# Kernel tuning notes

Hardware: AMD Instinct MI355X
Metric: run time of the kernel (lower is better)

Reference implementation:

```python
import jax, jax.numpy as jnp
import numpy as np

V = 50257   # vocab_size
E = 300     # embedding_dim
H2 = 1024   # hidden_size*2
CH = 6      # char_num
PMR = 32    # pmr_size
SX = 8192   # encoded_x seq len
SC = 4096   # encoded_con seq len
B = 1       # batch (decode step assumes b=1, see argmax/.item() in source)
S = 0.05    # weight init scale


def setup_inputs() -> dict:
    key = jax.random.key(0)
    ks = jax.random.split(key, 20)
    return {
        'input_idx': jax.random.randint(ks[0], (B,), 0, V),
        'encoded_x': jax.random.normal(ks[1], (B, SX, H2), jnp.float32),
        'encoded_con': jax.random.normal(ks[2], (B, SC, H2), jnp.float32),
        'p_matrix': jax.random.normal(ks[3], (B, CH * PMR, H2), jnp.float32),
        'hid': jax.random.normal(ks[4], (1, B, H2), jnp.float32),
        'c': jax.random.normal(ks[5], (1, B, H2), jnp.float32),
        'mask_x': jnp.ones((B, SX), bool),
        'mask_c': jnp.ones((B, SC), bool),
        # learned parameters
        'embed': jax.random.normal(ks[6], (V, E)) * S,
        'Wa': jax.random.normal(ks[7], (2 * H2, H2)) * S,   # Bahdanau attn proj
        'ba': jnp.zeros((H2,)),
        'va': jax.random.normal(ks[8], (H2,)) * S,
        'Wg': jax.random.normal(ks[9], (2 * H2, H2)) * S,   # fc_gate1
        'bg': jnp.zeros((H2,)),
        'Wchar': jax.random.normal(ks[10], (E + 2 * H2, CH)) * S,
        'bchar': jnp.zeros((CH,)),
        'Wp': jax.random.normal(ks[11], (H2, H2)) * S,       # w_p
        'bp': jnp.zeros((H2,)),
        'Wh': jax.random.normal(ks[12], (H2, H2)) * S,       # w_h
        'bh': jnp.zeros((H2,)),
        'vv': jax.random.normal(ks[13], (H2,)) * S,          # v (no bias)
        'Wy': jax.random.normal(ks[14], (E + 2 * H2, E)) * S,  # y_inp
        'by': jnp.zeros((E,)),
        'Wih': jax.random.normal(ks[15], (E, 4 * H2)) * S,   # LSTM input weights (i,f,g,o)
        'Whh': jax.random.normal(ks[16], (H2, 4 * H2)) * S,
        'bih': jnp.zeros((4 * H2,)),
        'bhh': jnp.zeros((4 * H2,)),
        'Wout': jax.random.normal(ks[17], (H2, V)) * S,      # out2
        'bout': jnp.zeros((V,)),
    }


def reference(input_idx, encoded_x, encoded_con, p_matrix, hid, c, mask_x, mask_c,
              embed, Wa, ba, va, Wg, bg, Wchar, bchar, Wp, bp, Wh, bh, vv,
              Wy, by, Wih, Whh, bih, bhh, Wout, bout):
    b = input_idx.shape[0]
    h0 = hid[0]                    # [b, 2h]
    c0 = c[0]
    y_input = embed[input_idx]     # [b, e] (dropout is identity at eval)

    def bahdanau(h, enc, mask):
        # h: [b,2h], enc: [b,seq,2h], mask: [b,seq] -> softmax weights [b,seq]
        hrep = jnp.broadcast_to(h[:, None, :], enc.shape)
        energy = jnp.tanh(jnp.concatenate([hrep, enc], -1) @ Wa + ba)  # [b,seq,2h]
        scores = energy @ va                                          # [b,seq]
        scores = jnp.where(mask, scores, -1e10)
        return jax.nn.softmax(scores, axis=1)

    a_x = bahdanau(h0, encoded_x, mask_x)
    weighted_x = jnp.einsum('bs,bsd->bd', a_x, encoded_x)
    a_c = bahdanau(h0, encoded_con, mask_c)
    weighted_c = jnp.einsum('bs,bsd->bd', a_c, encoded_con)
    weighted = jnp.concatenate([weighted_x, weighted_c], -1) @ Wg + bg  # [b,2h]

    # pointer: soft gate over chars -> hard one-hot selection -> gather rows of p_matrix
    g_char = jax.nn.softmax(jnp.concatenate([y_input, h0, weighted], -1) @ Wchar + bchar, axis=1)  # [b,6]
    pm = p_matrix.reshape(b, CH, -1)                       # [b,6,pmr*2h]
    nz = (pm.sum(axis=2) != 0).astype(g_char.dtype)
    z_char = g_char * nz
    o_char = jax.nn.one_hot(jnp.argmax(z_char, axis=1), CH, dtype=z_char.dtype)  # [b,6]
    s_char = (o_char[:, :, None] * pm).reshape(b, CH * PMR, H2)                  # [b,192,2h]

    # additive attention over the 192 selected slots (replicates source repeat/view layout, valid for b=1)
    hh = jnp.tile(h0, (CH * PMR, 1))                       # [192*b, 2h]
    pp = (s_char @ Wp + bp).reshape(-1, H2)                # [b*192, 2h]
    att = jnp.tanh(hh @ Wh + bh + pp) @ vv                 # [192*b]
    p_attn_score = jax.nn.softmax(att.reshape(b, -1), axis=1)     # [b,192]
    p_attn = jnp.einsum('bn,bnd->bd', p_attn_score, s_char)       # [b,2h]
    ps6 = p_attn_score.reshape(CH, -1)                            # [6, b*32]
    sel = jnp.argmax(o_char.reshape(-1))
    p_attn_score_sel = jnp.take(ps6, sel, axis=0)[None, :]        # [1, b*32]

    # LSTM cell step (torch gate order i,f,g,o)
    y_in = jnp.concatenate([y_input, weighted, p_attn], -1) @ Wy + by  # [b,e]
    gates = y_in @ Wih + bih + h0 @ Whh + bhh                          # [b,8h]
    gi, gf, gg, go = jnp.split(gates, 4, axis=1)
    c1 = jax.nn.sigmoid(gf) * c0 + jax.nn.sigmoid(gi) * jnp.tanh(gg)
    h1 = jax.nn.sigmoid(go) * jnp.tanh(c1)

    out = jax.nn.softmax(h1 @ Wout + bout, axis=1)[:, None, :]  # [b,1,vocab]
    return (out, h1[None], c1[None], weighted[:, None, :], p_attn_score_sel)
```

## Files before the change

kernel.cpp:

```cpp
#include <hip/hip_runtime.h>
#include <hip/hip_bf16.h>
#include <math.h>

typedef short short8 __attribute__((ext_vector_type(8)));
typedef float f32x4 __attribute__((ext_vector_type(4)));

#define DEV static __device__ __forceinline__

DEV void gl2lds16(const void* g, void* l) {
  __builtin_amdgcn_global_load_lds(
      (const __attribute__((address_space(1))) unsigned int*)g,
      (__attribute__((address_space(3))) unsigned int*)l, 16, 0, 0);
}

DEV float wred_sum(float v) {
#pragma unroll
  for (int o = 1; o < 64; o <<= 1) v += __shfl_xor(v, o, 64);
  return v;
}
DEV float wred_max(float v) {
#pragma unroll
  for (int o = 1; o < 64; o <<= 1) v = fmaxf(v, __shfl_xor(v, o, 64));
  return v;
}
DEV float sigmoidf(float x) { return 1.0f / (1.0f + expf(-x)); }

DEV unsigned short f2bf(float x) {
  unsigned u = __float_as_uint(x);
  unsigned rr = (u + 0x7fffu + ((u >> 16) & 1u)) >> 16;
  return (unsigned short)rr;
}

DEV short8 cvt8(float4 f0, float4 f1) {
  union { short8 s; unsigned u[4]; } r;
  asm("v_cvt_pk_bf16_f32 %0, %1, %2" : "=v"(r.u[0]) : "v"(f0.x), "v"(f0.y));
  asm("v_cvt_pk_bf16_f32 %0, %1, %2" : "=v"(r.u[1]) : "v"(f0.z), "v"(f0.w));
  asm("v_cvt_pk_bf16_f32 %0, %1, %2" : "=v"(r.u[2]) : "v"(f1.x), "v"(f1.y));
  asm("v_cvt_pk_bf16_f32 %0, %1, %2" : "=v"(r.u[3]) : "v"(f1.z), "v"(f1.w));
  return r.s;
}

#define OUT_H1 50257
#define OUT_C1 51281
#define OUT_W  52305
#define OUT_PS 53329

__global__ void k_prep_bT(const float* __restrict__ Wa, unsigned short* __restrict__ WaT) {
  __shared__ float tile[64][65];
  int bi = blockIdx.x, bj = blockIdx.y, t = threadIdx.x;
  int c = t & 63, rq = t >> 6;
#pragma unroll
  for (int rr = 0; rr < 16; rr++) {
    int kl = rr * 4 + rq;
    tile[kl][c] = Wa[(size_t)(1024 + bi * 64 + kl) * 1024 + bj * 64 + c];
  }
  __syncthreads();
#pragma unroll
  for (int rr = 0; rr < 16; rr++) {
    int nl = rr * 4 + rq;
    WaT[(size_t)(bj * 64 + nl) * 1024 + bi * 64 + c] = f2bf(tile[c][nl]);
  }
}

__global__ void k_prep_small(const float* __restrict__ Wa, const float* __restrict__ ba,
                             const float* __restrict__ Wh, const float* __restrict__ bh,
                             const float* __restrict__ hid, const float* __restrict__ embed,
                             const int* __restrict__ idx, const float* __restrict__ pmat,
                             float* __restrict__ hWa, float* __restrict__ hWh,
                             float* __restrict__ yinp, float* __restrict__ nz) {
  __shared__ float red[8][64];
  __shared__ float r2[8];
  int bx = blockIdx.x, t = threadIdx.x;
  if (bx < 32) {
    int ol = t & 63, kc = t >> 6;
    int o = bx * 64 + ol;
    const float* W = (o < 1024) ? Wa : Wh;
    int col = (o < 1024) ? o : (o - 1024);
    float acc = 0.f;
#pragma unroll 4
    for (int k = kc * 128; k < kc * 128 + 128; k++) acc += hid[k] * W[(size_t)k * 1024 + col];
    red[kc][ol] = acc;
    __syncthreads();
    if (t < 64) {
      int oo = bx * 64 + t;
      float s = 0.f;
#pragma unroll
      for (int q = 0; q < 8; q++) s += red[q][t];
      if (oo < 1024) hWa[oo] = s + ba[oo];
      else hWh[oo - 1024] = s + bh[oo - 1024];
    }
  } else if (bx == 32) {
    int id = idx[0];
    for (int k = t; k < 300; k += 512) yinp[k] = embed[(size_t)id * 300 + k];
  } else {
    int j = bx - 33;
    float a = 0.f;
    for (int k = t; k < 32768; k += 512) a += pmat[(size_t)j * 32768 + k];
    a = wred_sum(a);
    if ((t & 63) == 0) r2[t >> 6] = a;
    __syncthreads();
    if (t == 0) {
      float s = 0.f;
#pragma unroll
      for (int q = 0; q < 8; q++) s += r2[q];
      nz[j] = s;
    }
  }
}

__global__ __launch_bounds__(256) void k_scores_gemm(
    const float* __restrict__ ex, const float* __restrict__ ec,
    const unsigned short* __restrict__ WaT, const float* __restrict__ hWa,
    const float* __restrict__ va, float* __restrict__ scoresP) {
  __shared__ __align__(16) float As[128 * 32];
  __shared__ __align__(16) unsigned short Bs[128 * 32];
  __shared__ float red[2][128];
  int mtile = blockIdx.x, ntile = blockIdx.y;
  int t = threadIdx.x, lane = t & 63, wid = t >> 6;
  int wr = wid >> 1, wc = wid & 1;
  int l15 = lane & 15, lg = lane >> 4;
  int r0 = mtile * 128;
  const float* Asrc = (r0 < 8192) ? (ex + (size_t)r0 * 1024) : (ec + (size_t)(r0 - 8192) * 1024);

  f32x4 acc[4][4];
#pragma unroll
  for (int m = 0; m < 4; m++)
#pragma unroll
    for (int n = 0; n < 4; n++) acc[m][n] = (f32x4){0.f, 0.f, 0.f, 0.f};

  for (int kt = 0; kt < 1024; kt += 32) {
#pragma unroll
    for (int p = 0; p < 4; p++) {
      int cb = p * 256 + wid * 64;
      int c = cb + lane;
      const float* g = Asrc + (size_t)(c >> 3) * 1024 + kt + (c & 7) * 4;
      gl2lds16(g, &As[cb * 4]);
    }
#pragma unroll
    for (int p = 0; p < 2; p++) {
      int cb = p * 256 + wid * 64;
      int c = cb + lane;
      const unsigned short* g = WaT + (size_t)(ntile * 128 + (c >> 2)) * 1024 + kt + (c & 3) * 8;
      gl2lds16(g, &Bs[cb * 8]);
    }
    __syncthreads();
    short8 a[4], b[4];
#pragma unroll
    for (int m = 0; m < 4; m++) {
      const float* ap = &As[(wr * 64 + m * 16 + l15) * 32 + lg * 8];
      float4 f0 = *(const float4*)ap;
      float4 f1 = *(const float4*)(ap + 4);
      a[m] = cvt8(f0, f1);
    }
#pragma unroll
    for (int n = 0; n < 4; n++)
      b[n] = *(const short8*)&Bs[(wc * 64 + n * 16 + l15) * 32 + lg * 8];
#pragma unroll
    for (int m = 0; m < 4; m++)
#pragma unroll
      for (int n = 0; n < 4; n++)
        acc[m][n] = __builtin_amdgcn_mfma_f32_16x16x32_bf16(a[m], b[n], acc[m][n], 0, 0, 0);
    __syncthreads();
  }

  float vva[4], hba[4];
#pragma unroll
  for (int n = 0; n < 4; n++) {
    int col = ntile * 128 + wc * 64 + n * 16 + l15;
    vva[n] = va[col];
    hba[n] = hWa[col];
  }
#pragma unroll
  for (int m = 0; m < 4; m++) {
#pragma unroll
    for (int j = 0; j < 4; j++) {
      float p = 0.f;
#pragma unroll
      for (int n = 0; n < 4; n++) p += vva[n] * tanhf(acc[m][n][j] + hba[n]);
#pragma unroll
      for (int o = 1; o < 16; o <<= 1) p += __shfl_xor(p, o, 64);
      if (l15 == 0) red[wc][wr * 64 + m * 16 + lg * 4 + j] = p;
    }
  }
  __syncthreads();
  if (t < 128) scoresP[(size_t)ntile * 12288 + r0 + t] = red[0][t] + red[1][t];
}

__global__ void k_scores_reduce(const float* __restrict__ scoresP, float* __restrict__ scores,
                                float* __restrict__ bmax, float* __restrict__ bz) {
  __shared__ float r4[4];
  int bx = blockIdx.x, t = threadIdx.x;
  int r = bx * 256 + t;
  float s = 0.f;
#pragma unroll
  for (int nt = 0; nt < 8; nt++) s += scoresP[(size_t)nt * 12288 + r];
  scores[r] = s;
  float m = wred_max(s);
  if ((t & 63) == 0) r4[t >> 6] = m;
  __syncthreads();
  m = fmaxf(fmaxf(r4[0], r4[1]), fmaxf(r4[2], r4[3]));
  __syncthreads();
  float z = expf(s - m);
  z = wred_sum(z);
  if ((t & 63) == 0) r4[t >> 6] = z;
  __syncthreads();
  if (t == 0) { bmax[bx] = m; bz[bx] = r4[0] + r4[1] + r4[2] + r4[3]; }
}

__global__ void k_weighted_part(const float* __restrict__ ex, const float* __restrict__ ec,
                                const float* __restrict__ scores, const float* __restrict__ bmax,
                                const float* __restrict__ bz, float* __restrict__ partw) {
  __shared__ float wrow[64];
  int b = blockIdx.x, colq = blockIdx.y, t = threadIdx.x;
  int seg = (b >= 128) ? 1 : 0;
  int rb = (seg ? (b - 128) : b) * 64;
  int sbase = seg ? 8192 : 0;
  if (t < 64) {
    int b0 = seg ? 32 : 0, cnt = seg ? 16 : 32;
    float mv = (t < cnt) ? bmax[b0 + t] : -1e30f;
    float m = wred_max(mv);
    float zv = (t < cnt) ? bz[b0 + t] * expf(bmax[b0 + t] - m) : 0.f;
    float z = wred_sum(zv);
    wrow[t] = expf(scores[sbase + rb + t] - m) / z;
  }
  __syncthreads();
  const float* src = seg ? ec : ex;
  int col = colq * 256 + t;
  float acc = 0.f;
#pragma unroll 8
  for (int r = 0; r < 64; r++) acc += wrow[r] * src[(size_t)(rb + r) * 1024 + col];
  partw[(size_t)b * 1024 + col] = acc;
}

__global__ void k_weighted_combine(const float* __restrict__ partw, float* __restrict__ wxc) {
  int d = blockIdx.x * 256 + threadIdx.x;
  float sx = 0.f, sc = 0.f;
#pragma unroll 8
  for (int b = 0; b < 128; b++) sx += partw[(size_t)b * 1024 + d];
#pragma unroll 8
  for (int b = 128; b < 192; b++) sc += partw[(size_t)b * 1024 + d];
  wxc[d] = sx; wxc[1024 + d] = sc;
}

__global__ void k_weighted_gemv(const float* __restrict__ wxc, const float* __restrict__ Wg,
                                float* __restrict__ wgP) {
  int o = blockIdx.x * 256 + threadIdx.x;
  int kb = blockIdx.y * 64;
  float acc = 0.f;
#pragma unroll 8
  for (int k = kb; k < kb + 64; k++) acc += wxc[k] * Wg[(size_t)k * 1024 + o];
  wgP[(size_t)blockIdx.y * 1024 + o] = acc;
}

__global__ void k_wgfin_charsel(const float* __restrict__ wgP, const float* __restrict__ bg,
                                const float* __restrict__ yinp, const float* __restrict__ hid,
                                const float* __restrict__ Wchar, const float* __restrict__ bchar,
                                const float* __restrict__ nz, float* __restrict__ weighted,
                                int* __restrict__ sel, float* __restrict__ dout) {
  __shared__ float WL[1024];
  __shared__ float red[4][6];
  int t = threadIdx.x;
  for (int q = 0; q < 4; q++) {
    int d = t + q * 256;
    float s = bg[d];
#pragma unroll 8
    for (int b = 0; b < 32; b++) s += wgP[(size_t)b * 1024 + d];
    WL[d] = s;
    weighted[d] = s;
    dout[OUT_W + d] = s;
  }
  __syncthreads();
  float p[6] = {0.f, 0.f, 0.f, 0.f, 0.f, 0.f};
  for (int k = t; k < 2348; k += 256) {
    float xv = (k < 300) ? yinp[k] : (k < 1324 ? hid[k - 300] : WL[k - 1324]);
#pragma unroll
    for (int ch = 0; ch < 6; ch++) p[ch] += xv * Wchar[k * 6 + ch];
  }
#pragma unroll
  for (int ch = 0; ch < 6; ch++) {
    float v = wred_sum(p[ch]);
    if ((t & 63) == 0) red[t >> 6][ch] = v;
  }
  __syncthreads();
  if (t == 0) {
    float best = -1e30f; int si = 0;
    for (int ch = 0; ch < 6; ch++) {
      float lgt = red[0][ch] + red[1][ch] + red[2][ch] + red[3][ch] + bchar[ch];
      if (nz[ch] != 0.0f && lgt > best) { best = lgt; si = ch; }
    }
    *sel = si;
  }
}

__global__ void k_pp(const float* __restrict__ pmat, const float* __restrict__ Wp,
                     const int* __restrict__ sel, float* __restrict__ ppP) {
  __shared__ float sr[32][64];
  int oq = blockIdx.x, kq = blockIdx.y, t = threadIdx.x;
  int row0 = (*sel) * 32;
  int k0 = kq * 64;
#pragma unroll
  for (int j = 0; j < 8; j++) {
    int idx = t + j * 256;
    int i = idx >> 6, kk = idx & 63;
    sr[i][kk] = pmat[(size_t)(row0 + i) * 1024 + k0 + kk];
  }
  __syncthreads();
  int o = oq * 256 + t;
  float acc[32];
#pragma unroll
  for (int i = 0; i < 32; i++) acc[i] = 0.f;
  for (int k = 0; k < 64; k++) {
    float w = Wp[(size_t)(k0 + k) * 1024 + o];
#pragma unroll
    for (int i = 0; i < 32; i++) acc[i] += sr[i][k] * w;
  }
#pragma unroll
  for (int i = 0; i < 32; i++) ppP[(size_t)kq * 32768 + i * 1024 + o] = acc[i];
}

__global__ void k_pp_fin(const float* __restrict__ ppP, const float* __restrict__ bp,
                         float* __restrict__ pp) {
  int i = blockIdx.x, t = threadIdx.x;
  for (int q = 0; q < 4; q++) {
    int d = t + q * 256;
    float s = bp[d];
#pragma unroll
    for (int kq = 0; kq < 16; kq++) s += ppP[(size_t)kq * 32768 + i * 1024 + d];
    pp[i * 1024 + d] = s;
  }
}

__global__ void k_att(const float* __restrict__ pp, const float* __restrict__ hWh,
                      const float* __restrict__ bp, const float* __restrict__ vv,
                      float* __restrict__ attb) {
  __shared__ float r4[4];
  int i = blockIdx.x, t = threadIdx.x;
  const float* src = (i < 32) ? (pp + i * 1024) : bp;
  float pt = 0.f;
  for (int n = t; n < 1024; n += 256) pt += vv[n] * tanhf(hWh[n] + src[n]);
  pt = wred_sum(pt);
  if ((t & 63) == 0) r4[t >> 6] = pt;
  __syncthreads();
  if (t == 0) attb[i] = r4[0] + r4[1] + r4[2] + r4[3];
}

__global__ void k_pattn2(const float* __restrict__ attb, const float* __restrict__ pmat,
                         const int* __restrict__ sel, float* __restrict__ pattn,
                         float* __restrict__ dout) {
  __shared__ float sc32[32];
  int t = threadIdx.x, bx = blockIdx.x;
  if (t == 0) {
    float az = attb[32];
    float m = az;
    for (int i = 0; i < 32; i++) m = fmaxf(m, attb[i]);
    float Z = 160.0f * expf(az - m);
    for (int i = 0; i < 32; i++) Z += expf(attb[i] - m);
    for (int i = 0; i < 32; i++) sc32[i] = expf(attb[i] - m) / Z;
  }
  __syncthreads();
  if (bx == 0 && t < 32) dout[OUT_PS + t] = sc32[t];
  int d = bx * 256 + t;
  int srow0 = (*sel) * 32;
  float acc = 0.f;
#pragma unroll
  for (int i = 0; i < 32; i++) acc += sc32[i] * pmat[(size_t)(srow0 + i) * 1024 + d];
  pattn[d] = acc;
}

__global__ void k_yin_part(const float* __restrict__ yinp, const float* __restrict__ weighted,
                           const float* __restrict__ pattn, const float* __restrict__ Wy,
                           float* __restrict__ yinP) {
  __shared__ float XLb[74];
  int b = blockIdx.x, t = threadIdx.x;
  int base = b * 74;
  int len = 2348 - base; if (len > 74) len = 74;
  if (t < len) {
    int k = base + t;
    XLb[t] = (k < 300) ? yinp[k] : (k < 1324 ? weighted[k - 300] : pattn[k - 1324]);
  }
  __syncthreads();
  if (t < 300) {
    float acc = 0.f;
    for (int j = 0; j < len; j++) acc += XLb[j] * Wy[(size_t)(base + j) * 300 + t];
    yinP[b * 300 + t] = acc;
  }
}

__global__ void k_gates_part(const float* __restrict__ yinP, const float* __restrict__ by,
                             const float* __restrict__ hid,
                             const float* __restrict__ Wih, const float* __restrict__ Whh,
                             float* __restrict__ gatesP) {
  __shared__ float YLb[40];
  __shared__ float red[4][64];
  int bx = blockIdx.x, kq = blockIdx.y, t = threadIdx.x;
  int k0i = kq * 38;
  int k1i = k0i + 38; if (k1i > 300) k1i = 300;
  if (t < k1i - k0i) {
    float s = by[k0i + t];
#pragma unroll 8
    for (int b = 0; b < 32; b++) s += yinP[b * 300 + k0i + t];
    YLb[t] = s;
  }
  __syncthreads();
  int ol = t & 63, kc = t >> 6;
  int o = bx * 64 + ol;
  float acc = 0.f;
  for (int k = k0i + kc; k < k1i; k += 4) acc += YLb[k - k0i] * Wih[(size_t)k * 4096 + o];
  int kh0 = kq * 128;
#pragma unroll 4
  for (int k = kh0 + kc; k < kh0 + 128; k += 4) acc += hid[k] * Whh[(size_t)k * 4096 + o];
  red[kc][ol] = acc;
  __syncthreads();
  if (t < 64) {
    int oo = bx * 64 + t;
    gatesP[(size_t)kq * 4096 + oo] = red[0][t] + red[1][t] + red[2][t] + red[3][t];
  }
}

__global__ void k_lstm(const float* __restrict__ gatesP, const float* __restrict__ bih,
                       const float* __restrict__ bhh, const float* __restrict__ c0,
                       float* __restrict__ h1ws, float* __restrict__ dout) {
  int t = threadIdx.x;
  for (int q = 0; q < 4; q++) {
    int d = t + q * 256;
    float gi = bih[d] + bhh[d];
    float gf = bih[1024 + d] + bhh[1024 + d];
    float gg = bih[2048 + d] + bhh[2048 + d];
    float go = bih[3072 + d] + bhh[3072 + d];
#pragma unroll
    for (int kq = 0; kq < 8; kq++) {
      const float* g = gatesP + (size_t)kq * 4096;
      gi += g[d]; gf += g[1024 + d]; gg += g[2048 + d]; go += g[3072 + d];
    }
    float c1 = sigmoidf(gf) * c0[d] + sigmoidf(gi) * tanhf(gg);
    float h1 = sigmoidf(go) * tanhf(c1);
    h1ws[d] = h1;
    dout[OUT_H1 + d] = h1;
    dout[OUT_C1 + d] = c1;
  }
}

__global__ __launch_bounds__(256) void k_out_gemv(const float* __restrict__ h1,
                                                  const float* __restrict__ Wout,
                                                  float* __restrict__ partK) {
  __shared__ float hh[64];
  int ks = blockIdx.x, cb = blockIdx.y, t = threadIdx.x;
  if (t < 64) hh[t] = h1[ks * 64 + t];
  __syncthreads();
  int c0 = cb * 512 + t;
  int c1 = c0 + 256;
  bool v0 = c0 < 50257, v1 = c1 < 50257;
  float a0 = 0.f, a1 = 0.f;
  const float* W = Wout + (size_t)ks * 64 * 50257;
#pragma unroll 8
  for (int k = 0; k < 64; k++) {
    const float* row = W + (size_t)k * 50257;
    float h = hh[k];
    if (v0) a0 += h * row[c0];
    if (v1) a1 += h * row[c1];
  }
  float* dst = partK + (size_t)ks * 50257;
  if (v0) dst[c0] = a0;
  if (v1) dst[c1] = a1;
}

__global__ void k_logits_stats(const float* __restrict__ partK, const float* __restrict__ bout,
                               float* __restrict__ logits, float* __restrict__ bstat) {
  __shared__ float r4[4];
  int bx = blockIdx.x, t = threadIdx.x;
  int c = bx * 256 + t;
  float v = -1e30f;
  if (c < 50257) {
    v = bout[c];
#pragma unroll
    for (int ks = 0; ks < 16; ks++) v += partK[(size_t)ks * 50257 + c];
    logits[c] = v;
  }
  float m = wred_max(v);
  if ((t & 63) == 0) r4[t >> 6] = m;
  __syncthreads();
  m = fmaxf(fmaxf(r4[0], r4[1]), fmaxf(r4[2], r4[3]));
  __syncthreads();
  float z = (c < 50257) ? expf(v - m) : 0.f;
  z = wred_sum(z);
  if ((t & 63) == 0) r4[t >> 6] = z;
  __syncthreads();
  if (t == 0) { bstat[bx] = m; bstat[256 + bx] = r4[0] + r4[1] + r4[2] + r4[3]; }
}

__global__ void k_out_final(const float* __restrict__ bstat, const float* __restrict__ logits,
                            float* __restrict__ dout) {
  __shared__ float r4m[4], r4z[4];
  int bx = blockIdx.x, t = threadIdx.x;
  float mv = (t < 197) ? bstat[t] : -1e30f;
  float m = wred_max(mv);
  if ((t & 63) == 0) r4m[t >> 6] = m;
  __syncthreads();
  m = fmaxf(fmaxf(r4m[0], r4m[1]), fmaxf(r4m[2], r4m[3]));
  __syncthreads();
  float zv = (t < 197) ? bstat[256 + t] * expf(bstat[t] - m) : 0.f;
  float z = wred_sum(zv);
  if ((t & 63) == 0) r4z[t >> 6] = z;
  __syncthreads();
  float Z = r4z[0] + r4z[1] + r4z[2] + r4z[3];
  int c = bx * 256 + t;
  if (c < 50257) dout[c] = expf(logits[c] - m) / Z;
}

extern "C" void kernel_launch(void* const* d_in, const int* in_sizes, int n_in,
                              void* d_out, int out_size, void* d_ws, size_t ws_size,
                              hipStream_t stream) {
  (void)in_sizes; (void)n_in; (void)out_size; (void)ws_size;
  const int*   idx   = (const int*)  d_in[0];
  const float* ex    = (const float*)d_in[1];
  const float* ec    = (const float*)d_in[2];
  const float* pmat  = (const float*)d_in[3];
  const float* hid   = (const float*)d_in[4];
  const float* c0    = (const float*)d_in[5];
  const float* embed = (const float*)d_in[8];
  const float* Wa    = (const float*)d_in[9];
  const float* ba    = (const float*)d_in[10];
  const float* va    = (const float*)d_in[11];
  const float* Wg    = (const float*)d_in[12];
  const float* bg    = (const float*)d_in[13];
  const float* Wchar = (const float*)d_in[14];
  const float* bchar = (const float*)d_in[15];
  const float* Wp    = (const float*)d_in[16];
  const float* bp    = (const float*)d_in[17];
  const float* Wh    = (const float*)d_in[18];
  const float* bh    = (const float*)d_in[19];
  const float* vv    = (const float*)d_in[20];
  const float* Wy    = (const float*)d_in[21];
  const float* by    = (const float*)d_in[22];
  const float* Wih   = (const float*)d_in[23];
  const float* Whh   = (const float*)d_in[24];
  const float* bih   = (const float*)d_in[25];
  const float* bhh   = (const float*)d_in[26];
  const float* Wout  = (const float*)d_in[27];
  const float* bout  = (const float*)d_in[28];
  float* out = (float*)d_out;

  char* ws = (char*)d_ws;
  unsigned short* WaT = (unsigned short*)(ws + 0);
  float* scoresP  = (float*)(ws + 2097152);
  float* scores   = (float*)(ws + 2490368);
  float* bmax     = (float*)(ws + 2539520);
  float* bz       = (float*)(ws + 2539776);
  float* partw    = (float*)(ws + 2540032);
  float* wxc      = (float*)(ws + 3326464);
  float* wgP      = (float*)(ws + 3334656);
  float* partK    = (float*)(ws + 0);
  float* logits   = (float*)(ws + 3216640);
  float* pp       = (float*)(ws + 3465728);
  float* ppP      = (float*)(ws + 3596800);
  float* pattn    = (float*)(ws + 5693952);
  float* attb     = (float*)(ws + 5698048);
  float* yinP     = (float*)(ws + 5698304);
  float* gatesP   = (float*)(ws + 5736960);
  float* hWa      = (float*)(ws + 5868032);
  float* hWh      = (float*)(ws + 5872128);
  float* yinp     = (float*)(ws + 5876224);
  float* nz       = (float*)(ws + 5877760);
  float* weighted = (float*)(ws + 5878016);
  int*   sel      = (int*)  (ws + 5882112);
  float* h1       = (float*)(ws + 5882368);
  float* bstat    = (float*)(ws + 5886464);

  k_prep_bT<<<dim3(16, 16), 256, 0, stream>>>(Wa, WaT);
  k_prep_small<<<39, 512, 0, stream>>>(Wa, ba, Wh, bh, hid, embed, idx, pmat, hWa, hWh, yinp, nz);
  k_scores_gemm<<<dim3(96, 8), 256, 0, stream>>>(ex, ec, WaT, hWa, va, scoresP);
  k_scores_reduce<<<48, 256, 0, stream>>>(scoresP, scores, bmax, bz);
  k_weighted_part<<<dim3(192, 4), 256, 0, stream>>>(ex, ec, scores, bmax, bz, partw);
  k_weighted_combine<<<4, 256, 0, stream>>>(partw, wxc);
  k_weighted_gemv<<<dim3(4, 32), 256, 0, stream>>>(wxc, Wg, wgP);
  k_wgfin_charsel<<<1, 256, 0, stream>>>(wgP, bg, yinp, hid, Wchar, bchar, nz, weighted, sel, out);
  k_pp<<<dim3(4, 16), 256, 0, stream>>>(pmat, Wp, sel, ppP);
  k_pp_fin<<<32, 256, 0, stream>>>(ppP, bp, pp);
  k_att<<<33, 256, 0, stream>>>(pp, hWh, bp, vv, attb);
  k_pattn2<<<4, 256, 0, stream>>>(attb, pmat, sel, pattn, out);
  k_yin_part<<<32, 320, 0, stream>>>(yinp, weighted, pattn, Wy, yinP);
  k_gates_part<<<dim3(64, 8), 256, 0, stream>>>(yinP, by, hid, Wih, Whh, gatesP);
  k_lstm<<<1, 256, 0, stream>>>(gatesP, bih, bhh, c0, h1, out);
  k_out_gemv<<<dim3(16, 100), 256, 0, stream>>>(h1, Wout, partK);
  k_logits_stats<<<197, 256, 0, stream>>>(partK, bout, logits, bstat);
  k_out_final<<<197, 256, 0, stream>>>(bstat, logits, out);
}
```

Baseline: 272.9 us.

## Pre-convert encoder states to bf16, widen GEMM K-tile with swizzled LDS, vectorize gemvs

A new kernel converts encoded_x and encoded_con to bf16 once. The scores GEMM and the weighted-sum pass then read half the bytes, and the GEMM skips per-tile fp32-to-bf16 conversion. The scores GEMM now uses a 64-wide K tile with an XOR-swizzled LDS layout to cut bank conflicts. The weighted sum now uses bf16 encoder values instead of fp32, which lowers precision. The output gemv is vectorized to 4 columns per thread with a padded partial stride, and the pp finalize and attention kernels are fused into one. The extra conversion pass costs a full read of the fp32 encoders plus a bf16 write, and the workspace grows by about 25 MB.

Result: faster. 258.2 us (-5.4%).

```diff
diff --git a/kernel.cpp b/kernel.cpp
--- a/kernel.cpp
+++ b/kernel.cpp
@@ -4,6 +4,7 @@
 
 typedef short short8 __attribute__((ext_vector_type(8)));
 typedef float f32x4 __attribute__((ext_vector_type(4)));
+typedef float f32x4u __attribute__((ext_vector_type(4), aligned(4)));
 
 #define DEV static __device__ __forceinline__
 
@@ -44,6 +45,17 @@
 #define OUT_C1 51281
 #define OUT_W  52305
 #define OUT_PS 53329
+#define PKS 50260
+
+__global__ __launch_bounds__(256) void k_enc_bf16(const float* __restrict__ ex,
+                                                  const float* __restrict__ ec,
+                                                  unsigned short* __restrict__ encb) {
+  size_t i = ((size_t)blockIdx.x * 256 + threadIdx.x) * 8;
+  const float* src = (i < 8388608) ? (ex + i) : (ec + (i - 8388608));
+  float4 f0 = *(const float4*)src;
+  float4 f1 = *(const float4*)(src + 4);
+  *(short8*)&encb[i] = cvt8(f0, f1);
+}
 
 __global__ void k_prep_bT(const float* __restrict__ Wa, unsigned short* __restrict__ WaT) {
   __shared__ float tile[64][65];
@@ -109,18 +121,17 @@
 }
 
 __global__ __launch_bounds__(256) void k_scores_gemm(
-    const float* __restrict__ ex, const float* __restrict__ ec,
-    const unsigned short* __restrict__ WaT, const float* __restrict__ hWa,
-    const float* __restrict__ va, float* __restrict__ scoresP) {
-  __shared__ __align__(16) float As[128 * 32];
-  __shared__ __align__(16) unsigned short Bs[128 * 32];
+    const unsigned short* __restrict__ encb, const unsigned short* __restrict__ WaT,
+    const float* __restrict__ hWa, const float* __restrict__ va,
+    float* __restrict__ scoresP) {
+  __shared__ __align__(16) unsigned short As[128 * 64];
+  __shared__ __align__(16) unsigned short Bs[128 * 64];
   __shared__ float red[2][128];
   int mtile = blockIdx.x, ntile = blockIdx.y;
   int t = threadIdx.x, lane = t & 63, wid = t >> 6;
   int wr = wid >> 1, wc = wid & 1;
   int l15 = lane & 15, lg = lane >> 4;
   int r0 = mtile * 128;
-  const float* Asrc = (r0 < 8192) ? (ex + (size_t)r0 * 1024) : (ec + (size_t)(r0 - 8192) * 1024);
 
   f32x4 acc[4][4];
 #pragma unroll
@@ -128,38 +139,44 @@
 #pragma unroll
     for (int n = 0; n < 4; n++) acc[m][n] = (f32x4){0.f, 0.f, 0.f, 0.f};
 
-  for (int kt = 0; kt < 1024; kt += 32) {
+  for (int kt = 0; kt < 1024; kt += 64) {
 #pragma unroll
     for (int p = 0; p < 4; p++) {
-      int cb = p * 256 + wid * 64;
-      int c = cb + lane;
-      const float* g = Asrc + (size_t)(c >> 3) * 1024 + kt + (c & 7) * 4;
-      gl2lds16(g, &As[cb * 4]);
-    }
-#pragma unroll
-    for (int p = 0; p < 2; p++) {
-      int cb = p * 256 + wid * 64;
-      int c = cb + lane;
-      const unsigned short* g = WaT + (size_t)(ntile * 128 + (c >> 2)) * 1024 + kt + (c & 3) * 8;
-      gl2lds16(g, &Bs[cb * 8]);
+      int c = p * 256 + t;
+      int row = c >> 3, slot = c & 7;
+      const unsigned short* g =
+          encb + (size_t)(r0 + row) * 1024 + kt + ((slot ^ (row & 7)) * 8);
+      gl2lds16(g, &As[c * 8]);
+    }
+#pragma unroll
+    for (int p = 0; p < 4; p++) {
+      int c = p * 256 + t;
+      int row = c >> 3, slot = c & 7;
+      const unsigned short* g =
+          WaT + (size_t)(ntile * 128 + row) * 1024 + kt + ((slot ^ (row & 7)) * 8);
+      gl2lds16(g, &Bs[c * 8]);
     }
     __syncthreads();
-    short8 a[4], b[4];
-#pragma unroll
-    for (int m = 0; m < 4; m++) {
-      const float* ap = &As[(wr * 64 + m * 16 + l15) * 32 + lg * 8];
-      float4 f0 = *(const float4*)ap;
-      float4 f1 = *(const float4*)(ap + 4);
-      a[m] = cvt8(f0, f1);
-    }
-#pragma unroll
-    for (int n = 0; n < 4; n++)
-      b[n] = *(const short8*)&Bs[(wc * 64 + n * 16 + l15) * 32 + lg * 8];
-#pragma unroll
-    for (int m = 0; m < 4; m++)
-#pragma unroll
-      for (int n = 0; n < 4; n++)
-        acc[m][n] = __builtin_amdgcn_mfma_f32_16x16x32_bf16(a[m], b[n], acc[m][n], 0, 0, 0);
+#pragma unroll
+    for (int ks = 0; ks < 2; ks++) {
+      short8 a[4], b[4];
+      int q = ks * 4 + lg;
+#pragma unroll
+      for (int m = 0; m < 4; m++) {
+        int row = wr * 64 + m * 16 + l15;
+        a[m] = *(const short8*)&As[row * 64 + ((q ^ (row & 7)) * 8)];
+      }
+#pragma unroll
+      for (int n = 0; n < 4; n++) {
+        int nr = wc * 64 + n * 16 + l15;
+        b[n] = *(const short8*)&Bs[nr * 64 + ((q ^ (nr & 7)) * 8)];
+      }
+#pragma unroll
+      for (int m = 0; m < 4; m++)
+#pragma unroll
+        for (int n = 0; n < 4; n++)
+          acc[m][n] = __builtin_amdgcn_mfma_f32_16x16x32_bf16(a[m], b[n], acc[m][n], 0, 0, 0);
+    }
     __syncthreads();
   }
 
@@ -207,14 +224,14 @@
   if (t == 0) { bmax[bx] = m; bz[bx] = r4[0] + r4[1] + r4[2] + r4[3]; }
 }
 
-__global__ void k_weighted_part(const float* __restrict__ ex, const float* __restrict__ ec,
+__global__ void k_weighted_part(const unsigned short* __restrict__ encb,
                                 const float* __restrict__ scores, const float* __restrict__ bmax,
                                 const float* __restrict__ bz, float* __restrict__ partw) {
   __shared__ float wrow[64];
   int b = blockIdx.x, colq = blockIdx.y, t = threadIdx.x;
   int seg = (b >= 128) ? 1 : 0;
-  int rb = (seg ? (b - 128) : b) * 64;
   int sbase = seg ? 8192 : 0;
+  int rb = seg ? (b - 128) * 64 : b * 64;
   if (t < 64) {
     int b0 = seg ? 32 : 0, cnt = seg ? 16 : 32;
     float mv = (t < cnt) ? bmax[b0 + t] : -1e30f;
@@ -224,12 +241,18 @@
     wrow[t] = expf(scores[sbase + rb + t] - m) / z;
   }
   __syncthreads();
-  const float* src = seg ? ec : ex;
-  int col = colq * 256 + t;
-  float acc = 0.f;
+  int c2 = colq * 512 + 2 * t;
+  float a0 = 0.f, a1 = 0.f;
+  size_t rowbase = (size_t)b * 64 * 1024;
 #pragma unroll 8
-  for (int r = 0; r < 64; r++) acc += wrow[r] * src[(size_t)(rb + r) * 1024 + col];
-  partw[(size_t)b * 1024 + col] = acc;
+  for (int r = 0; r < 64; r++) {
+    unsigned u = *(const unsigned*)&encb[rowbase + (size_t)r * 1024 + c2];
+    float w = wrow[r];
+    a0 += w * __uint_as_float(u << 16);
+    a1 += w * __uint_as_float(u & 0xffff0000u);
+  }
+  float2 o; o.x = a0; o.y = a1;
+  *(float2*)&partw[(size_t)b * 1024 + c2] = o;
 }
 
 __global__ void k_weighted_combine(const float* __restrict__ partw, float* __restrict__ wxc) {
@@ -318,26 +341,27 @@
   for (int i = 0; i < 32; i++) ppP[(size_t)kq * 32768 + i * 1024 + o] = acc[i];
 }
 
-__global__ void k_pp_fin(const float* __restrict__ ppP, const float* __restrict__ bp,
-                         float* __restrict__ pp) {
-  int i = blockIdx.x, t = threadIdx.x;
-  for (int q = 0; q < 4; q++) {
-    int d = t + q * 256;
-    float s = bp[d];
-#pragma unroll
-    for (int kq = 0; kq < 16; kq++) s += ppP[(size_t)kq * 32768 + i * 1024 + d];
-    pp[i * 1024 + d] = s;
-  }
-}
-
-__global__ void k_att(const float* __restrict__ pp, const float* __restrict__ hWh,
-                      const float* __restrict__ bp, const float* __restrict__ vv,
-                      float* __restrict__ attb) {
+__global__ void k_ppfin_att(const float* __restrict__ ppP, const float* __restrict__ bp,
+                            const float* __restrict__ hWh, const float* __restrict__ vv,
+                            float* __restrict__ pp, float* __restrict__ attb) {
   __shared__ float r4[4];
   int i = blockIdx.x, t = threadIdx.x;
-  const float* src = (i < 32) ? (pp + i * 1024) : bp;
   float pt = 0.f;
-  for (int n = t; n < 1024; n += 256) pt += vv[n] * tanhf(hWh[n] + src[n]);
+  if (i < 32) {
+    for (int q = 0; q < 4; q++) {
+      int d = t + q * 256;
+      float s = bp[d];
+#pragma unroll
+      for (int kq = 0; kq < 16; kq++) s += ppP[(size_t)kq * 32768 + i * 1024 + d];
+      pp[i * 1024 + d] = s;
+      pt += vv[d] * tanhf(hWh[d] + s);
+    }
+  } else {
+    for (int q = 0; q < 4; q++) {
+      int d = t + q * 256;
+      pt += vv[d] * tanhf(hWh[d] + bp[d]);
+    }
+  }
   pt = wred_sum(pt);
   if ((t & 63) == 0) r4[t >> 6] = pt;
   __syncthreads();
@@ -447,21 +471,25 @@
   int ks = blockIdx.x, cb = blockIdx.y, t = threadIdx.x;
   if (t < 64) hh[t] = h1[ks * 64 + t];
   __syncthreads();
-  int c0 = cb * 512 + t;
-  int c1 = c0 + 256;
-  bool v0 = c0 < 50257, v1 = c1 < 50257;
-  float a0 = 0.f, a1 = 0.f;
   const float* W = Wout + (size_t)ks * 64 * 50257;
+  int c4 = cb * 1024 + t * 4;
+  if (c4 + 4 <= 50257) {
+    f32x4 a = (f32x4){0.f, 0.f, 0.f, 0.f};
+#pragma unroll 4
+    for (int k = 0; k < 64; k++) {
+      f32x4u w = *(const f32x4u*)&W[(size_t)k * 50257 + c4];
+      float h = hh[k];
+      a[0] += h * w[0]; a[1] += h * w[1]; a[2] += h * w[2]; a[3] += h * w[3];
+    }
+    *(f32x4*)&partK[(size_t)ks * PKS + c4] = a;
+  } else if (c4 < 50257) {
+    for (int c = c4; c < 50257; c++) {
+      float a = 0.f;
 #pragma unroll 8
-  for (int k = 0; k < 64; k++) {
-    const float* row = W + (size_t)k * 50257;
-    float h = hh[k];
-    if (v0) a0 += h * row[c0];
-    if (v1) a1 += h * row[c1];
-  }
-  float* dst = partK + (size_t)ks * 50257;
-  if (v0) dst[c0] = a0;
-  if (v1) dst[c1] = a1;
+      for (int k = 0; k < 64; k++) a += hh[k] * W[(size_t)k * 50257 + c];
+      partK[(size_t)ks * PKS + c] = a;
+    }
+  }
 }
 
 __global__ void k_logits_stats(const float* __restrict__ partK, const float* __restrict__ bout,
@@ -473,7 +501,7 @@
   if (c < 50257) {
     v = bout[c];
 #pragma unroll
-    for (int ks = 0; ks < 16; ks++) v += partK[(size_t)ks * 50257 + c];
+    for (int ks = 0; ks < 16; ks++) v += partK[(size_t)ks * PKS + c];
     logits[c] = v;
   }
   float m = wred_max(v);
@@ -541,47 +569,48 @@
   float* out = (float*)d_out;
 
   char* ws = (char*)d_ws;
-  unsigned short* WaT = (unsigned short*)(ws + 0);
-  float* scoresP  = (float*)(ws + 2097152);
-  float* scores   = (float*)(ws + 2490368);
-  float* bmax     = (float*)(ws + 2539520);
-  float* bz       = (float*)(ws + 2539776);
-  float* partw    = (float*)(ws + 2540032);
-  float* wxc      = (float*)(ws + 3326464);
-  float* wgP      = (float*)(ws + 3334656);
+  unsigned short* encb = (unsigned short*)(ws + 0);
+  unsigned short* WaT  = (unsigned short*)(ws + 25165824);
+  float* scoresP  = (float*)(ws + 27262976);
+  float* scores   = (float*)(ws + 27656192);
+  float* bmax     = (float*)(ws + 27705344);
+  float* bz       = (float*)(ws + 27705600);
+  float* partw    = (float*)(ws + 27705856);
+  float* wxc      = (float*)(ws + 28492288);
+  float* wgP      = (float*)(ws + 28500480);
   float* partK    = (float*)(ws + 0);
   float* logits   = (float*)(ws + 3216640);
-  float* pp       = (float*)(ws + 3465728);
-  float* ppP      = (float*)(ws + 3596800);
-  float* pattn    = (float*)(ws + 5693952);
-  float* attb     = (float*)(ws + 5698048);
-  float* yinP     = (float*)(ws + 5698304);
-  float* gatesP   = (float*)(ws + 5736960);
-  float* hWa      = (float*)(ws + 5868032);
-  float* hWh      = (float*)(ws + 5872128);
-  float* yinp     = (float*)(ws + 5876224);
-  float* nz       = (float*)(ws + 5877760);
-  float* weighted = (float*)(ws + 5878016);
-  int*   sel      = (int*)  (ws + 5882112);
-  float* h1       = (float*)(ws + 5882368);
-  float* bstat    = (float*)(ws + 5886464);
-
+  float* pp       = (float*)(ws + 28631552);
+  float* ppP      = (float*)(ws + 28762624);
+  float* pattn    = (float*)(ws + 30859776);
+  float* attb     = (float*)(ws + 30863872);
+  float* yinP     = (float*)(ws + 30864128);
+  float* gatesP   = (float*)(ws + 30902784);
+  float* hWa      = (float*)(ws + 31033856);
+  float* hWh      = (float*)(ws + 31037952);
+  float* yinp     = (float*)(ws + 31042048);
+  float* nz       = (float*)(ws + 31043584);
+  float* weighted = (float*)(ws + 31043840);
+  int*   sel      = (int*)  (ws + 31047936);
+  float* h1       = (float*)(ws + 31048192);
+  float* bstat    = (float*)(ws + 31052288);
+
+  k_enc_bf16<<<6144, 256, 0, stream>>>(ex, ec, encb);
   k_prep_bT<<<dim3(16, 16), 256, 0, stream>>>(Wa, WaT);
   k_prep_small<<<39, 512, 0, stream>>>(Wa, ba, Wh, bh, hid, embed, idx, pmat, hWa, hWh, yinp, nz);
-  k_scores_gemm<<<dim3(96, 8), 256, 0, stream>>>(ex, ec, WaT, hWa, va, scoresP);
+  k_scores_gemm<<<dim3(96, 8), 256, 0, stream>>>(encb, WaT, hWa, va, scoresP);
   k_scores_reduce<<<48, 256, 0, stream>>>(scoresP, scores, bmax, bz);
-  k_weighted_part<<<dim3(192, 4), 256, 0, stream>>>(ex, ec, scores, bmax, bz, partw);
+  k_weighted_part<<<dim3(192, 2), 256, 0, stream>>>(encb, scores, bmax, bz, partw);
   k_weighted_combine<<<4, 256, 0, stream>>>(partw, wxc);
   k_weighted_gemv<<<dim3(4, 32), 256, 0, stream>>>(wxc, Wg, wgP);
   k_wgfin_charsel<<<1, 256, 0, stream>>>(wgP, bg, yinp, hid, Wchar, bchar, nz, weighted, sel, out);
   k_pp<<<dim3(4, 16), 256, 0, stream>>>(pmat, Wp, sel, ppP);
-  k_pp_fin<<<32, 256, 0, stream>>>(ppP, bp, pp);
-  k_att<<<33, 256, 0, stream>>>(pp, hWh, bp, vv, attb);
+  k_ppfin_att<<<33, 256, 0, stream>>>(ppP, bp, hWh, vv, pp, attb);
   k_pattn2<<<4, 256, 0, stream>>>(attb, pmat, sel, pattn, out);
   k_yin_part<<<32, 320, 0, stream>>>(yinp, weighted, pattn, Wy, yinP);
   k_gates_part<<<dim3(64, 8), 256, 0, stream>>>(yinP, by, hid, Wih, Whh, gatesP);
   k_lstm<<<1, 256, 0, stream>>>(gatesP, bih, bhh, c0, h1, out);
-  k_out_gemv<<<dim3(16, 100), 256, 0, stream>>>(h1, Wout, partK);
+  k_out_gemv<<<dim3(16, 50), 256, 0, stream>>>(h1, Wout, partK);
   k_logits_stats<<<197, 256, 0, stream>>>(partK, bout, logits, bstat);
   k_out_final<<<197, 256, 0, stream>>>(bstat, logits, out);
 }
```
